# Performance work log

Measured on AMD Instinct MI355X. Metric: run time of the kernel, lower is better.

The kernel has to match this reference:

```python
import jax, jax.numpy as jnp
import numpy as np

EMBED_DIM = 768
NUM_HEADS = 12
HEAD_DIM = EMBED_DIM // NUM_HEADS
SEGMENT_LENGTHS = [2048, 4096, 8192]
DILATION_RATES = [1, 2, 4]
SCALE = 1.0 / np.sqrt(HEAD_DIM)
B, S = 1, 8192


def setup_inputs() -> dict:
    key = jax.random.key(0)
    ks = jax.random.split(key, 5)
    std = 1.0 / np.sqrt(EMBED_DIM)
    return {
        "x": jax.random.normal(ks[0], (B, S, EMBED_DIM), dtype=jnp.float32),
        "Wqkv": jax.random.normal(ks[1], (EMBED_DIM, 3 * EMBED_DIM), dtype=jnp.float32) * std,
        "bqkv": jax.random.normal(ks[2], (3 * EMBED_DIM,), dtype=jnp.float32) * 0.01,
        "Wout": jax.random.normal(ks[3], (EMBED_DIM, EMBED_DIM), dtype=jnp.float32) * std,
        "bout": jax.random.normal(ks[4], (EMBED_DIM,), dtype=jnp.float32) * 0.01,
    }


def _attend(q, k, v):
    # q,k,v: [B,H,L,D]; full softmax attention (non-causal)
    scores = jnp.einsum("bhqd,bhkd->bhqk", q, k) * SCALE
    w = jax.nn.softmax(scores, axis=-1)
    return jnp.einsum("bhqk,bhkd->bhqd", w, v)


def reference(x, Wqkv, bqkv, Wout, bout):
    b, s, _ = x.shape
    qkv = x @ Wqkv + bqkv                                  # [B,S,3E]
    qkv = qkv.reshape(b, s, 3, NUM_HEADS, HEAD_DIM)
    qkv = jnp.transpose(qkv, (2, 0, 3, 1, 4))              # [3,B,H,S,D]
    q, k, v = qkv[0], qkv[1], qkv[2]

    outputs = []
    for seg_len, dil in zip(SEGMENT_LENGTHS, DILATION_RATES):
        if seg_len > s:
            continue
        if dil > 1:
            idx = np.arange(0, s, dil)[:seg_len]           # static indices
            seg_out = _attend(q[:, :, idx, :], k[:, :, idx, :], v[:, :, idx, :])
            full = jnp.zeros((b, NUM_HEADS, s, HEAD_DIM), dtype=seg_out.dtype)
            full = full.at[:, :, idx, :].set(seg_out)
        else:
            seg_out = _attend(q[:, :, :seg_len, :], k[:, :, :seg_len, :], v[:, :, :seg_len, :])
            pad = s - seg_out.shape[2]
            full = jnp.pad(seg_out, ((0, 0), (0, 0), (0, pad), (0, 0))) if pad > 0 else seg_out
        outputs.append(full)

    out = jnp.mean(jnp.stack(outputs), axis=0) if len(outputs) > 1 else outputs[0]
    out = jnp.transpose(out, (0, 2, 1, 3)).reshape(b, s, EMBED_DIM)
    return out @ Wout + bout
```

## Files before the change

kernel.cpp:

```cpp
#include <hip/hip_runtime.h>
#include <hip/hip_bf16.h>

typedef float f32x4 __attribute__((ext_vector_type(4)));
typedef float fvec4 __attribute__((ext_vector_type(4)));
typedef __bf16 bf16x8 __attribute__((ext_vector_type(8)));
typedef __bf16 bf16x2 __attribute__((ext_vector_type(2)));

__device__ inline float fexp2(float x) {
#if __has_builtin(__builtin_amdgcn_exp2f)
    return __builtin_amdgcn_exp2f(x);
#else
    return exp2f(x);
#endif
}

__device__ __forceinline__ bf16x2 pk_bf16(float a, float b) {
#if __has_builtin(__builtin_amdgcn_cvt_pk_bf16_f32)
    auto t = __builtin_amdgcn_cvt_pk_bf16_f32(a, b);
    return __builtin_bit_cast(bf16x2, t);
#else
    bf16x2 r; r[0] = (__bf16)a; r[1] = (__bf16)b; return r;
#endif
}

#define MFMA_BF16(a, b, c) __builtin_amdgcn_mfma_f32_16x16x32_bf16((a), (b), (c), 0, 0, 0)

__device__ __forceinline__ void gl2lds16(const void* g, void* l) {
    __builtin_amdgcn_global_load_lds((const __attribute__((address_space(1))) void*)g,
                                     (__attribute__((address_space(3))) void*)l, 16, 0, 0);
}

#define SEG1OFF ((size_t)12 * 2048 * 64)
#define SEG2OFF ((size_t)12 * 6144 * 64)
#define QSCALE 0.18033688f

__global__ __launch_bounds__(256) void prep_kernel(
    const float* __restrict__ x, const float* __restrict__ Wqkv,
    const float* __restrict__ Wout, __bf16* __restrict__ xb,
    __bf16* __restrict__ WqkvT, __bf16* __restrict__ WoutT) {
    int bid = blockIdx.x, tid = threadIdx.x;
    if (bid < 3072) {
        int i = bid * 256 + tid;
        fvec4 a = ((const fvec4*)x)[2 * i];
        fvec4 b = ((const fvec4*)x)[2 * i + 1];
        bf16x8 o;
        o[0] = (__bf16)a[0]; o[1] = (__bf16)a[1]; o[2] = (__bf16)a[2]; o[3] = (__bf16)a[3];
        o[4] = (__bf16)b[0]; o[5] = (__bf16)b[1]; o[6] = (__bf16)b[2]; o[7] = (__bf16)b[3];
        ((bf16x8*)xb)[i] = o;
    } else if (bid < 3936) {
        int b = bid - 3072;
        int n = (b % 9) * 256 + tid;
        int kg = b / 9;
        bf16x8 o;
#pragma unroll
        for (int j = 0; j < 8; j++) o[j] = (__bf16)Wqkv[(size_t)(kg * 8 + j) * 2304 + n];
        *(bf16x8*)&WqkvT[(size_t)n * 768 + kg * 8] = o;
    } else {
        int b = bid - 3936;
        int n = (b % 3) * 256 + tid;
        int kg = b / 3;
        bf16x8 o;
#pragma unroll
        for (int j = 0; j < 8; j++) o[j] = (__bf16)Wout[(size_t)(kg * 8 + j) * 768 + n];
        *(bf16x8*)&WoutT[(size_t)n * 768 + kg * 8] = o;
    }
}

__global__ __launch_bounds__(256) void vtrans_kernel(const __bf16* __restrict__ Vc,
                                                     __bf16* __restrict__ Vt) {
    __shared__ __bf16 T[64][68];
    int bid = blockIdx.x;
    int Lc, head, t;
    size_t soff;
    if (bid < 768)       { Lc = 4096; head = bid >> 6; t = bid & 63; soff = SEG1OFF; }
    else if (bid < 1152) { int i = bid - 768; Lc = 2048; head = i >> 5; t = i & 31; soff = 0; }
    else                 { int i = bid - 1152; Lc = 2048; head = i >> 5; t = i & 31; soff = SEG2OFF; }
    const __bf16* src = Vc + soff + (size_t)head * Lc * 64;
    __bf16* dst = Vt + soff + (size_t)head * 64 * Lc;
    int tid = threadIdx.x;
#pragma unroll
    for (int it = 0; it < 2; it++) {
        int s = tid + it * 256;
        int kvr = s >> 3, d8 = (s & 7) * 8;
        bf16x8 vv = *(const bf16x8*)&src[(size_t)(t * 64 + kvr) * 64 + d8];
#pragma unroll
        for (int j = 0; j < 8; j++) T[d8 + j][kvr] = vv[j];
    }
    __syncthreads();
#pragma unroll
    for (int it = 0; it < 2; it++) {
        int s = tid + it * 256;
        int d = s >> 3, ck = s & 7;
        int kb = (ck >> 2) * 32 + (ck & 3) * 4;
        bf16x8 o;
#pragma unroll
        for (int J = 0; J < 8; J++) o[J] = T[d][kb + (J & 3) + (J >> 2) * 16];
        *(bf16x8*)&dst[(size_t)d * Lc + t * 64 + ck * 8] = o;
    }
}

__global__ __launch_bounds__(256, 2) void gemm_qkv_kernel(
    const __bf16* __restrict__ Ab, const __bf16* __restrict__ Bt,
    const float* __restrict__ bias,
    __bf16* __restrict__ Qc, __bf16* __restrict__ Kc, __bf16* __restrict__ Vc) {
    __shared__ __align__(16) char smem[65536];
    __bf16* T = (__bf16*)smem;
    int tid = threadIdx.x;
    int wave = tid >> 6, lane = tid & 63;
    int quad = lane >> 4, l15 = lane & 15;
    int bm = blockIdx.x * 128, bn = blockIdx.y * 128;
    int wm = (wave >> 1) * 64, wn = (wave & 1) * 64;
    int swzA = tid & 7;
    int rows_[4], chs_[4];
#pragma unroll
    for (int j = 0; j < 4; j++) {
        int s = j * 256 + tid;
        rows_[j] = s >> 3;
        chs_[j] = swzA ^ (rows_[j] & 7);
    }
    f32x4 acc[4][4] = {};
    {
#pragma unroll
        for (int j = 0; j < 4; j++) {
            gl2lds16(&Ab[(size_t)(bm + rows_[j]) * 768 + chs_[j] * 8],
                     smem + j * 4096 + wave * 1024);
            gl2lds16(&Bt[(size_t)(bn + rows_[j]) * 768 + chs_[j] * 8],
                     smem + 16384 + j * 4096 + wave * 1024);
        }
    }
    for (int ki = 0; ki < 12; ki++) {
        __syncthreads();
        int cur = ki & 1;
        if (ki + 1 < 12) {
            int nb = (cur ^ 1) * 32768;
            int k1 = (ki + 1) * 64;
#pragma unroll
            for (int j = 0; j < 4; j++) {
                gl2lds16(&Ab[(size_t)(bm + rows_[j]) * 768 + k1 + chs_[j] * 8],
                         smem + nb + j * 4096 + wave * 1024);
                gl2lds16(&Bt[(size_t)(bn + rows_[j]) * 768 + k1 + chs_[j] * 8],
                         smem + nb + 16384 + j * 4096 + wave * 1024);
            }
        }
        const __bf16* Al = (const __bf16*)(smem + cur * 32768);
        const __bf16* Bl = Al + 8192;
#pragma unroll
        for (int ks = 0; ks < 2; ks++) {
            bf16x8 af[4], bfr[4];
#pragma unroll
            for (int i = 0; i < 4; i++) {
                int row = wm + i * 16 + l15;
                af[i] = *(const bf16x8*)&Al[row * 64 + (((ks * 4 + quad) ^ (row & 7)) * 8)];
            }
#pragma unroll
            for (int j = 0; j < 4; j++) {
                int row = wn + j * 16 + l15;
                bfr[j] = *(const bf16x8*)&Bl[row * 64 + (((ks * 4 + quad) ^ (row & 7)) * 8)];
            }
#pragma unroll
            for (int i = 0; i < 4; i++)
#pragma unroll
                for (int j = 0; j < 4; j++)
                    acc[i][j] = MFMA_BF16(af[i], bfr[j], acc[i][j]);
        }
    }
    int which = blockIdx.y / 6;
    int h0 = (blockIdx.y % 6) * 2;
    float scl = which == 0 ? QSCALE : 1.0f;
    float bv[4];
#pragma unroll
    for (int j = 0; j < 4; j++) bv[j] = bias[bn + wn + j * 16 + l15];
    __syncthreads();
#pragma unroll
    for (int i = 0; i < 4; i++)
#pragma unroll
        for (int j = 0; j < 4; j++) {
            int col = wn + j * 16 + l15;
#pragma unroll
            for (int r = 0; r < 4; r++) {
                int row = wm + i * 16 + quad * 4 + r;
                int ch = ((col >> 3) & 8) | (((col >> 3) & 7) ^ (row & 7));
                T[row * 136 + ch * 8 + (col & 7)] =
                    (__bf16)((acc[i][j][r] + bv[j]) * scl);
            }
        }
    __syncthreads();
    __bf16* dst = which == 0 ? Qc : (which == 1 ? Kc : Vc);
    int rr = tid >> 4;
    int c8 = tid & 15;
    int hh = c8 >> 3, d8 = c8 & 7;
    int h = h0 + hh;
    __bf16* p0 = dst + ((size_t)h * 2048 * 64) + d8 * 8;
    __bf16* p1 = dst + SEG1OFF + ((size_t)h * 4096 * 64) + d8 * 8;
    __bf16* p2 = dst + SEG2OFF + ((size_t)h * 2048 * 64) + d8 * 8;
#pragma unroll
    for (int pass = 0; pass < 8; pass++) {
        int row = pass * 16 + rr;
        int pos = bm + row;
        int ch = (c8 & 8) | ((c8 & 7) ^ (row & 7));
        bf16x8 v = *(const bf16x8*)&T[row * 136 + ch * 8];
        if (pos < 2048) *(bf16x8*)&p0[(size_t)pos * 64] = v;
        if (!(pos & 1)) *(bf16x8*)&p1[(size_t)(pos >> 1) * 64] = v;
        if (!(pos & 3)) *(bf16x8*)&p2[(size_t)(pos >> 2) * 64] = v;
    }
}

__global__ __launch_bounds__(256) void gemm_out_kernel(
    const __bf16* __restrict__ Ab, const __bf16* __restrict__ Bt,
    const float* __restrict__ bias, float* __restrict__ Co) {
    __shared__ __align__(16) char smem[49152];
    int tid = threadIdx.x;
    int wave = tid >> 6, lane = tid & 63;
    int quad = lane >> 4, l15 = lane & 15;
    int bm = blockIdx.x * 64, bn = blockIdx.y * 128;
    int wn = wave * 32;
    int rowsA[2], chsA[2], rowsB[4], chsB[4];
#pragma unroll
    for (int j = 0; j < 2; j++) {
        int s = j * 256 + tid;
        rowsA[j] = s >> 3;
        chsA[j] = (s & 7) ^ (rowsA[j] & 7);
    }
#pragma unroll
    for (int j = 0; j < 4; j++) {
        int s = j * 256 + tid;
        rowsB[j] = s >> 3;
        chsB[j] = (s & 7) ^ (rowsB[j] & 7);
    }
    f32x4 acc[4][2] = {};
    {
#pragma unroll
        for (int j = 0; j < 2; j++)
            gl2lds16(&Ab[(size_t)(bm + rowsA[j]) * 768 + chsA[j] * 8],
                     smem + j * 4096 + wave * 1024);
#pragma unroll
        for (int j = 0; j < 4; j++)
            gl2lds16(&Bt[(size_t)(bn + rowsB[j]) * 768 + chsB[j] * 8],
                     smem + 8192 + j * 4096 + wave * 1024);
    }
    for (int ki = 0; ki < 12; ki++) {
        __syncthreads();
        int cur = ki & 1;
        if (ki + 1 < 12) {
            int nb = (cur ^ 1) * 24576;
            int k1 = (ki + 1) * 64;
#pragma unroll
            for (int j = 0; j < 2; j++)
                gl2lds16(&Ab[(size_t)(bm + rowsA[j]) * 768 + k1 + chsA[j] * 8],
                         smem + nb + j * 4096 + wave * 1024);
#pragma unroll
            for (int j = 0; j < 4; j++)
                gl2lds16(&Bt[(size_t)(bn + rowsB[j]) * 768 + k1 + chsB[j] * 8],
                         smem + nb + 8192 + j * 4096 + wave * 1024);
        }
        const __bf16* Al = (const __bf16*)(smem + cur * 24576);
        const __bf16* Bl = Al + 4096;
#pragma unroll
        for (int ks = 0; ks < 2; ks++) {
            bf16x8 af[4], bfr[2];
#pragma unroll
            for (int i = 0; i < 4; i++) {
                int row = i * 16 + l15;
                af[i] = *(const bf16x8*)&Al[row * 64 + (((ks * 4 + quad) ^ (row & 7)) * 8)];
            }
#pragma unroll
            for (int j = 0; j < 2; j++) {
                int row = wn + j * 16 + l15;
                bfr[j] = *(const bf16x8*)&Bl[row * 64 + (((ks * 4 + quad) ^ (row & 7)) * 8)];
            }
#pragma unroll
            for (int i = 0; i < 4; i++)
#pragma unroll
                for (int j = 0; j < 2; j++)
                    acc[i][j] = MFMA_BF16(af[i], bfr[j], acc[i][j]);
        }
    }
#pragma unroll
    for (int j = 0; j < 2; j++) {
        int c = bn + wn + j * 16 + l15;
        float bv = bias[c];
#pragma unroll
        for (int i = 0; i < 4; i++)
#pragma unroll
            for (int r = 0; r < 4; r++) {
                int row = bm + i * 16 + quad * 4 + r;
                Co[(size_t)row * 768 + c] = acc[i][j][r] + bv;
            }
    }
}

__global__ __launch_bounds__(256, 2) void attn_kernel(
    const __bf16* __restrict__ Qcb, const __bf16* __restrict__ Kcb,
    const __bf16* __restrict__ Vtb,
    float* __restrict__ O0, float* __restrict__ O1a, float* __restrict__ O1b,
    float* __restrict__ O1c, float* __restrict__ O1d, float* __restrict__ O2,
    float* __restrict__ L0, float* __restrict__ L1a, float* __restrict__ L1b,
    float* __restrict__ L1c, float* __restrict__ L1d, float* __restrict__ L2) {
    __shared__ __bf16 Kl[2 * 4096];
    __shared__ __bf16 Vl[2 * 4096];
    int bid = blockIdx.x;
    int seg, piece = 0, head, qt, Lc, iters;
    if (bid < 192)      { seg = 0; head = bid >> 4; qt = bid & 15; Lc = 2048; iters = 32; }
    else if (bid < 384) { int i = bid - 192; seg = 2; head = i >> 4; qt = i & 15; Lc = 2048; iters = 32; }
    else                { int i = bid - 384; seg = 1; head = i >> 7; int r = i & 127;
                          qt = r >> 2; piece = r & 3; Lc = 4096; iters = 16; }
    size_t soff = seg == 0 ? 0 : (seg == 1 ? SEG1OFF : SEG2OFF);
    const __bf16* Qh = Qcb + soff + (size_t)head * Lc * 64;
    const __bf16* Kh = Kcb + soff + (size_t)head * Lc * 64;
    const __bf16* Vh = Vtb + soff + (size_t)head * 64 * Lc;
    float* Ob;
    float* Lb;
    if (seg == 0)      { Ob = O0; Lb = L0 + head * 2048; }
    else if (seg == 2) { Ob = O2; Lb = L2 + head * 2048; }
    else {
        Ob = piece == 0 ? O1a : (piece == 1 ? O1b : (piece == 2 ? O1c : O1d));
        Lb = (piece == 0 ? L1a : (piece == 1 ? L1b : (piece == 2 ? L1c : L1d))) + head * 4096;
    }
    int kvb = piece * 16;
    int tid = threadIdx.x, wave = tid >> 6, lane = tid & 63;
    int quad = lane >> 4, l15 = lane & 15;
    bf16x8 qf[2][2];
#pragma unroll
    for (int qg = 0; qg < 2; qg++) {
        size_t qpos = (size_t)(qt * 128 + wave * 32 + qg * 16 + l15);
        qf[qg][0] = *(const bf16x8*)&Qh[qpos * 64 + quad * 8];
        qf[qg][1] = *(const bf16x8*)&Qh[qpos * 64 + 32 + quad * 8];
    }
    f32x4 o[2][4] = {};
    f32x4 lacc[2] = {};
    bf16x8 ones;
#pragma unroll
    for (int j = 0; j < 8; j++) ones[j] = (__bf16)1.0f;
    int kv0 = tid >> 3, cl0 = tid & 7;
    int kdb0 = cl0 ^ (kv0 & 7);
    int kv1 = kv0 + 32, kdb1 = cl0 ^ (kv1 & 7);
    char* KlB = (char*)Kl;
    char* VlB = (char*)Vl;
    int swz = l15 & 7;
    {
        int t0 = kvb * 64;
        gl2lds16(&Kh[(size_t)(t0 + kv0) * 64 + kdb0 * 8], KlB + wave * 1024);
        gl2lds16(&Kh[(size_t)(t0 + kv1) * 64 + kdb1 * 8], KlB + 4096 + wave * 1024);
        gl2lds16(&Vh[(size_t)kv0 * Lc + t0 + kdb0 * 8], VlB + wave * 1024);
        gl2lds16(&Vh[(size_t)kv1 * Lc + t0 + kdb1 * 8], VlB + 4096 + wave * 1024);
    }
    for (int nt = 0; nt < iters; nt++) {
        __syncthreads();
        int cur = nt & 1;
        if (nt + 1 < iters) {
            int nb = 8192 * (cur ^ 1);
            int t1 = (kvb + nt + 1) * 64;
            gl2lds16(&Kh[(size_t)(t1 + kv0) * 64 + kdb0 * 8], KlB + nb + wave * 1024);
            gl2lds16(&Kh[(size_t)(t1 + kv1) * 64 + kdb1 * 8], KlB + nb + 4096 + wave * 1024);
            gl2lds16(&Vh[(size_t)kv0 * Lc + t1 + kdb0 * 8], VlB + nb + wave * 1024);
            gl2lds16(&Vh[(size_t)kv1 * Lc + t1 + kdb1 * 8], VlB + nb + 4096 + wave * 1024);
        }
        const __bf16* Kt = Kl + cur * 4096;
        const __bf16* Vt_ = Vl + cur * 4096;
        f32x4 sarr[4][2];
#pragma unroll
        for (int c = 0; c < 4; c++) {
            int krow = (c * 16 + l15) * 64;
            bf16x8 kf0 = *(const bf16x8*)&Kt[krow + ((quad ^ swz) * 8)];
            bf16x8 kf1 = *(const bf16x8*)&Kt[krow + (((4 + quad) ^ swz) * 8)];
#pragma unroll
            for (int qg = 0; qg < 2; qg++) {
                f32x4 z = {};
                z = MFMA_BF16(kf0, qf[qg][0], z);
                sarr[c][qg] = MFMA_BF16(kf1, qf[qg][1], z);
            }
        }
        union { bf16x8 v8; bf16x2 v2[4]; } pf8[2][2];
#pragma unroll
        for (int qg = 0; qg < 2; qg++)
#pragma unroll
            for (int c = 0; c < 4; c++) {
                float p0 = fexp2(sarr[c][qg][0]);
                float p1 = fexp2(sarr[c][qg][1]);
                float p2 = fexp2(sarr[c][qg][2]);
                float p3 = fexp2(sarr[c][qg][3]);
                pf8[qg][c >> 1].v2[(c & 1) * 2 + 0] = pk_bf16(p0, p1);
                pf8[qg][c >> 1].v2[(c & 1) * 2 + 1] = pk_bf16(p2, p3);
            }
#pragma unroll
        for (int u = 0; u < 2; u++) {
#pragma unroll
            for (int ds = 0; ds < 4; ds++) {
                int d = ds * 16 + l15;
                bf16x8 vf = *(const bf16x8*)&Vt_[d * 64 + (((u * 4 + quad) ^ swz) * 8)];
                o[0][ds] = MFMA_BF16(vf, pf8[0][u].v8, o[0][ds]);
                o[1][ds] = MFMA_BF16(vf, pf8[1][u].v8, o[1][ds]);
            }
            lacc[0] = MFMA_BF16(ones, pf8[0][u].v8, lacc[0]);
            lacc[1] = MFMA_BF16(ones, pf8[1][u].v8, lacc[1]);
        }
    }
#pragma unroll
    for (int qg = 0; qg < 2; qg++) {
        float l = lacc[qg][0];
        int pos = qt * 128 + wave * 32 + qg * 16 + l15;
        float* orow = Ob + (size_t)pos * 768 + head * 64;
#pragma unroll
        for (int ds = 0; ds < 4; ds++)
            *(f32x4*)&orow[ds * 16 + quad * 4] = o[qg][ds];
        if (lane < 16) Lb[qt * 128 + wave * 32 + qg * 16 + lane] = l;
    }
}

__global__ __launch_bounds__(256) void combine_kernel(
    const float* __restrict__ O0, const float* __restrict__ O1a,
    const float* __restrict__ O1b, const float* __restrict__ O1c,
    const float* __restrict__ O1d, const float* __restrict__ O2,
    const float* __restrict__ L0, const float* __restrict__ L1a,
    const float* __restrict__ L1b, const float* __restrict__ L1c,
    const float* __restrict__ L1d, const float* __restrict__ L2,
    __bf16* __restrict__ attnF) {
    int g = blockIdx.x * 256 + threadIdx.x;
    int q = g / 96;
    int cs = (g - q * 96) * 8;
    int head = cs >> 6;
    f32x4 a0 = {}, a1 = {};
    if (q < 2048) {
        float inv = 1.0f / L0[head * 2048 + q];
        const f32x4* p = (const f32x4*)&O0[(size_t)q * 768 + cs];
        a0 += p[0] * inv; a1 += p[1] * inv;
    }
    if (!(q & 1)) {
        int p1 = q >> 1;
        int li = head * 4096 + p1;
        float inv = 1.0f / (L1a[li] + L1b[li] + L1c[li] + L1d[li]);
        size_t ro = (size_t)p1 * 768 + cs;
        const f32x4* pa = (const f32x4*)&O1a[ro];
        const f32x4* pb = (const f32x4*)&O1b[ro];
        const f32x4* pc = (const f32x4*)&O1c[ro];
        const f32x4* pd = (const f32x4*)&O1d[ro];
        a0 += ((pa[0] + pb[0]) + (pc[0] + pd[0])) * inv;
        a1 += ((pa[1] + pb[1]) + (pc[1] + pd[1])) * inv;
    }
    if (!(q & 3)) {
        int p2 = q >> 2;
        float inv = 1.0f / L2[head * 2048 + p2];
        const f32x4* p = (const f32x4*)&O2[(size_t)p2 * 768 + cs];
        a0 += p[0] * inv; a1 += p[1] * inv;
    }
    const float third = 1.0f / 3.0f;
    bf16x8 ov;
    ov[0] = (__bf16)(a0[0] * third); ov[1] = (__bf16)(a0[1] * third);
    ov[2] = (__bf16)(a0[2] * third); ov[3] = (__bf16)(a0[3] * third);
    ov[4] = (__bf16)(a1[0] * third); ov[5] = (__bf16)(a1[1] * third);
    ov[6] = (__bf16)(a1[2] * third); ov[7] = (__bf16)(a1[3] * third);
    *(bf16x8*)&attnF[(size_t)q * 768 + cs] = ov;
}

extern "C" void kernel_launch(void* const* d_in, const int* in_sizes, int n_in,
                              void* d_out, int out_size, void* d_ws, size_t ws_size,
                              hipStream_t stream) {
    const float* x    = (const float*)d_in[0];
    const float* Wqkv = (const float*)d_in[1];
    const float* bqkv = (const float*)d_in[2];
    const float* Wout = (const float*)d_in[3];
    const float* bout = (const float*)d_in[4];
    float* out = (float*)d_out;
    (void)in_sizes; (void)n_in; (void)out_size; (void)ws_size;

    char* ws = (char*)d_ws;
    size_t off = 0;
    auto take = [&](size_t bytes) -> void* {
        void* p = ws + off;
        off += (bytes + 255) & ~(size_t)255;
        return p;
    };
    const size_t QKV_ELEMS = (size_t)12 * 8192 * 64;
    __bf16* xb    = (__bf16*)take((size_t)8192 * 768 * 2);
    __bf16* WqkvT = (__bf16*)take((size_t)2304 * 768 * 2);
    __bf16* WoutT = (__bf16*)take((size_t)768 * 768 * 2);
    __bf16* Qc    = (__bf16*)take(QKV_ELEMS * 2);
    __bf16* Kc    = (__bf16*)take(QKV_ELEMS * 2);
    __bf16* Vc    = (__bf16*)take(QKV_ELEMS * 2);
    __bf16* Vt    = (__bf16*)take(QKV_ELEMS * 2);
    float*  O1a   = (float*)take((size_t)4096 * 768 * 4);
    float*  O1b   = (float*)take((size_t)4096 * 768 * 4);
    float*  O1c   = (float*)take((size_t)4096 * 768 * 4);
    float*  L0    = (float*)take((size_t)12 * 2048 * 4);
    float*  L1a   = (float*)take((size_t)12 * 4096 * 4);
    float*  L1b   = (float*)take((size_t)12 * 4096 * 4);
    float*  L1c   = (float*)take((size_t)12 * 4096 * 4);
    float*  L1d   = (float*)take((size_t)12 * 4096 * 4);
    float*  L2    = (float*)take((size_t)12 * 2048 * 4);
    float*  O0    = (float*)xb;
    float*  O2    = O0 + (size_t)2048 * 768;
    float*  O1d   = (float*)Vc;
    __bf16* attnF = Qc;

    prep_kernel<<<4224, 256, 0, stream>>>(x, Wqkv, Wout, xb, WqkvT, WoutT);
    gemm_qkv_kernel<<<dim3(64, 18), 256, 0, stream>>>(xb, WqkvT, bqkv, Qc, Kc, Vc);
    vtrans_kernel<<<1536, 256, 0, stream>>>(Vc, Vt);
    attn_kernel<<<1920, 256, 0, stream>>>(Qc, Kc, Vt, O0, O1a, O1b, O1c, O1d, O2,
                                          L0, L1a, L1b, L1c, L1d, L2);
    combine_kernel<<<3072, 256, 0, stream>>>(O0, O1a, O1b, O1c, O1d, O2,
                                             L0, L1a, L1b, L1c, L1d, L2, attnF);
    gemm_out_kernel<<<dim3(128, 6), 256, 0, stream>>>(attnF, WoutT, bout, out);
}
```

Baseline: 239.1 us.

## Halve segment-1 KV split and hand-schedule attention loop waits and barriers

Segment-1 attention now splits the KV range into two pieces instead of four, so every block runs 32 iterations. This cuts the grid from 1920 to 1152 blocks, drops two partial O/L buffers, and lightens the combine kernel's reads. The attention loop replaces __syncthreads with explicit vmcnt waits, s_barrier and sched_barrier fences so the next tile's K/V prefetch can stay in flight across the QK and exp phases, and raises wave priority around the MFMA sections. The risks are less parallelism in segment 1 and a hand-counted vmcnt scheme that depends on how the compiler orders the memory ops.

```diff
diff --git a/kernel.cpp b/kernel.cpp
--- a/kernel.cpp
+++ b/kernel.cpp
@@ -24,6 +24,7 @@
 }
 
 #define MFMA_BF16(a, b, c) __builtin_amdgcn_mfma_f32_16x16x32_bf16((a), (b), (c), 0, 0, 0)
+#define SCHED_FENCE() __builtin_amdgcn_sched_barrier(0)
 
 __device__ __forceinline__ void gl2lds16(const void* g, void* l) {
     __builtin_amdgcn_global_load_lds((const __attribute__((address_space(1))) void*)g,
@@ -293,17 +294,17 @@
     const __bf16* __restrict__ Qcb, const __bf16* __restrict__ Kcb,
     const __bf16* __restrict__ Vtb,
     float* __restrict__ O0, float* __restrict__ O1a, float* __restrict__ O1b,
-    float* __restrict__ O1c, float* __restrict__ O1d, float* __restrict__ O2,
+    float* __restrict__ O2,
     float* __restrict__ L0, float* __restrict__ L1a, float* __restrict__ L1b,
-    float* __restrict__ L1c, float* __restrict__ L1d, float* __restrict__ L2) {
+    float* __restrict__ L2) {
     __shared__ __bf16 Kl[2 * 4096];
     __shared__ __bf16 Vl[2 * 4096];
     int bid = blockIdx.x;
-    int seg, piece = 0, head, qt, Lc, iters;
-    if (bid < 192)      { seg = 0; head = bid >> 4; qt = bid & 15; Lc = 2048; iters = 32; }
-    else if (bid < 384) { int i = bid - 192; seg = 2; head = i >> 4; qt = i & 15; Lc = 2048; iters = 32; }
-    else                { int i = bid - 384; seg = 1; head = i >> 7; int r = i & 127;
-                          qt = r >> 2; piece = r & 3; Lc = 4096; iters = 16; }
+    int seg, piece = 0, head, qt, Lc;
+    if (bid < 192)      { seg = 0; head = bid >> 4; qt = bid & 15; Lc = 2048; }
+    else if (bid < 384) { int i = bid - 192; seg = 2; head = i >> 4; qt = i & 15; Lc = 2048; }
+    else                { int i = bid - 384; seg = 1; head = i >> 6; int r = i & 63;
+                          qt = r >> 1; piece = r & 1; Lc = 4096; }
     size_t soff = seg == 0 ? 0 : (seg == 1 ? SEG1OFF : SEG2OFF);
     const __bf16* Qh = Qcb + soff + (size_t)head * Lc * 64;
     const __bf16* Kh = Kcb + soff + (size_t)head * Lc * 64;
@@ -312,11 +313,8 @@
     float* Lb;
     if (seg == 0)      { Ob = O0; Lb = L0 + head * 2048; }
     else if (seg == 2) { Ob = O2; Lb = L2 + head * 2048; }
-    else {
-        Ob = piece == 0 ? O1a : (piece == 1 ? O1b : (piece == 2 ? O1c : O1d));
-        Lb = (piece == 0 ? L1a : (piece == 1 ? L1b : (piece == 2 ? L1c : L1d))) + head * 4096;
-    }
-    int kvb = piece * 16;
+    else               { Ob = piece ? O1b : O1a; Lb = (piece ? L1b : L1a) + head * 4096; }
+    int kvb = piece * 32;
     int tid = threadIdx.x, wave = tid >> 6, lane = tid & 63;
     int quad = lane >> 4, l15 = lane & 15;
     bf16x8 qf[2][2];
@@ -341,23 +339,30 @@
         int t0 = kvb * 64;
         gl2lds16(&Kh[(size_t)(t0 + kv0) * 64 + kdb0 * 8], KlB + wave * 1024);
         gl2lds16(&Kh[(size_t)(t0 + kv1) * 64 + kdb1 * 8], KlB + 4096 + wave * 1024);
+        SCHED_FENCE();
         gl2lds16(&Vh[(size_t)kv0 * Lc + t0 + kdb0 * 8], VlB + wave * 1024);
         gl2lds16(&Vh[(size_t)kv1 * Lc + t0 + kdb1 * 8], VlB + 4096 + wave * 1024);
     }
-    for (int nt = 0; nt < iters; nt++) {
-        __syncthreads();
+    for (int nt = 0; nt < 32; nt++) {
         int cur = nt & 1;
-        if (nt + 1 < iters) {
+        SCHED_FENCE();
+        asm volatile("s_waitcnt vmcnt(2)" ::: "memory");
+        __builtin_amdgcn_s_barrier();
+        SCHED_FENCE();
+        if (nt + 1 < 32) {
             int nb = 8192 * (cur ^ 1);
             int t1 = (kvb + nt + 1) * 64;
             gl2lds16(&Kh[(size_t)(t1 + kv0) * 64 + kdb0 * 8], KlB + nb + wave * 1024);
             gl2lds16(&Kh[(size_t)(t1 + kv1) * 64 + kdb1 * 8], KlB + nb + 4096 + wave * 1024);
+            SCHED_FENCE();
             gl2lds16(&Vh[(size_t)kv0 * Lc + t1 + kdb0 * 8], VlB + nb + wave * 1024);
             gl2lds16(&Vh[(size_t)kv1 * Lc + t1 + kdb1 * 8], VlB + nb + 4096 + wave * 1024);
         }
+        SCHED_FENCE();
         const __bf16* Kt = Kl + cur * 4096;
         const __bf16* Vt_ = Vl + cur * 4096;
         f32x4 sarr[4][2];
+        __builtin_amdgcn_s_setprio(1);
 #pragma unroll
         for (int c = 0; c < 4; c++) {
             int krow = (c * 16 + l15) * 64;
@@ -370,6 +375,7 @@
                 sarr[c][qg] = MFMA_BF16(kf1, qf[qg][1], z);
             }
         }
+        __builtin_amdgcn_s_setprio(0);
         union { bf16x8 v8; bf16x2 v2[4]; } pf8[2][2];
 #pragma unroll
         for (int qg = 0; qg < 2; qg++)
@@ -382,6 +388,15 @@
                 pf8[qg][c >> 1].v2[(c & 1) * 2 + 0] = pk_bf16(p0, p1);
                 pf8[qg][c >> 1].v2[(c & 1) * 2 + 1] = pk_bf16(p2, p3);
             }
+        SCHED_FENCE();
+        if (nt + 1 < 32) {
+            asm volatile("s_waitcnt vmcnt(4)" ::: "memory");
+        } else {
+            asm volatile("s_waitcnt vmcnt(0)" ::: "memory");
+        }
+        __builtin_amdgcn_s_barrier();
+        SCHED_FENCE();
+        __builtin_amdgcn_s_setprio(1);
 #pragma unroll
         for (int u = 0; u < 2; u++) {
 #pragma unroll
@@ -394,6 +409,7 @@
             lacc[0] = MFMA_BF16(ones, pf8[0][u].v8, lacc[0]);
             lacc[1] = MFMA_BF16(ones, pf8[1][u].v8, lacc[1]);
         }
+        __builtin_amdgcn_s_setprio(0);
     }
 #pragma unroll
     for (int qg = 0; qg < 2; qg++) {
@@ -409,11 +425,9 @@
 
 __global__ __launch_bounds__(256) void combine_kernel(
     const float* __restrict__ O0, const float* __restrict__ O1a,
-    const float* __restrict__ O1b, const float* __restrict__ O1c,
-    const float* __restrict__ O1d, const float* __restrict__ O2,
+    const float* __restrict__ O1b, const float* __restrict__ O2,
     const float* __restrict__ L0, const float* __restrict__ L1a,
-    const float* __restrict__ L1b, const float* __restrict__ L1c,
-    const float* __restrict__ L1d, const float* __restrict__ L2,
+    const float* __restrict__ L1b, const float* __restrict__ L2,
     __bf16* __restrict__ attnF) {
     int g = blockIdx.x * 256 + threadIdx.x;
     int q = g / 96;
@@ -428,14 +442,12 @@
     if (!(q & 1)) {
         int p1 = q >> 1;
         int li = head * 4096 + p1;
-        float inv = 1.0f / (L1a[li] + L1b[li] + L1c[li] + L1d[li]);
+        float inv = 1.0f / (L1a[li] + L1b[li]);
         size_t ro = (size_t)p1 * 768 + cs;
         const f32x4* pa = (const f32x4*)&O1a[ro];
         const f32x4* pb = (const f32x4*)&O1b[ro];
-        const f32x4* pc = (const f32x4*)&O1c[ro];
-        const f32x4* pd = (const f32x4*)&O1d[ro];
-        a0 += ((pa[0] + pb[0]) + (pc[0] + pd[0])) * inv;
-        a1 += ((pa[1] + pb[1]) + (pc[1] + pd[1])) * inv;
+        a0 += (pa[0] + pb[0]) * inv;
+        a1 += (pa[1] + pb[1]) * inv;
     }
     if (!(q & 3)) {
         int p2 = q >> 2;
@@ -479,25 +491,21 @@
     __bf16* Vc    = (__bf16*)take(QKV_ELEMS * 2);
     __bf16* Vt    = (__bf16*)take(QKV_ELEMS * 2);
     float*  O1a   = (float*)take((size_t)4096 * 768 * 4);
-    float*  O1b   = (float*)take((size_t)4096 * 768 * 4);
-    float*  O1c   = (float*)take((size_t)4096 * 768 * 4);
     float*  L0    = (float*)take((size_t)12 * 2048 * 4);
     float*  L1a   = (float*)take((size_t)12 * 4096 * 4);
     float*  L1b   = (float*)take((size_t)12 * 4096 * 4);
-    float*  L1c   = (float*)take((size_t)12 * 4096 * 4);
-    float*  L1d   = (float*)take((size_t)12 * 4096 * 4);
     float*  L2    = (float*)take((size_t)12 * 2048 * 4);
     float*  O0    = (float*)xb;
     float*  O2    = O0 + (size_t)2048 * 768;
-    float*  O1d   = (float*)Vc;
+    float*  O1b   = (float*)Vc;
     __bf16* attnF = Qc;
 
     prep_kernel<<<4224, 256, 0, stream>>>(x, Wqkv, Wout, xb, WqkvT, WoutT);
     gemm_qkv_kernel<<<dim3(64, 18), 256, 0, stream>>>(xb, WqkvT, bqkv, Qc, Kc, Vc);
     vtrans_kernel<<<1536, 256, 0, stream>>>(Vc, Vt);
-    attn_kernel<<<1920, 256, 0, stream>>>(Qc, Kc, Vt, O0, O1a, O1b, O1c, O1d, O2,
-                                          L0, L1a, L1b, L1c, L1d, L2);
-    combine_kernel<<<3072, 256, 0, stream>>>(O0, O1a, O1b, O1c, O1d, O2,
-                                             L0, L1a, L1b, L1c, L1d, L2, attnF);
+    attn_kernel<<<1152, 256, 0, stream>>>(Qc, Kc, Vt, O0, O1a, O1b, O2,
+                                          L0, L1a, L1b, L2);
+    combine_kernel<<<3072, 256, 0, stream>>>(O0, O1a, O1b, O2,
+                                             L0, L1a, L1b, L2, attnF);
     gemm_out_kernel<<<dim3(128, 6), 256, 0, stream>>>(attnF, WoutT, bout, out);
 }
```

Measured after the change: 241.0 us. Within noise of the previous version (+0.8%).
